# Optimization experiments

Hardware: AMD Instinct MI355X
Metric: run time of the kernel (lower is better)

Reference implementation:

```python
import jax, jax.numpy as jnp
import numpy as np

N_FEATURES = 60
WINDOW = 64
N_FFT_BINS = WINDOW // 2 + 1  # 33
HIDDEN = 256
N_OUT = 3
TOTAL_IN = N_FEATURES + N_FEATURES * N_FFT_BINS  # 2040


def setup_inputs() -> dict:
    key = jax.random.key(0)
    ks = jax.random.split(key, 9)
    B, T = 4, 4096
    x = jax.random.normal(ks[0], (B, T, N_FEATURES), dtype=jnp.float32)

    def lin(k, fan_in, fan_out):
        bound = 1.0 / np.sqrt(fan_in)
        kw, kb = jax.random.split(k)
        W = jax.random.uniform(kw, (fan_in, fan_out), minval=-bound, maxval=bound, dtype=jnp.float32)
        b = jax.random.uniform(kb, (fan_out,), minval=-bound, maxval=bound, dtype=jnp.float32)
        return W, b

    W1, b1 = lin(ks[1], TOTAL_IN, HIDDEN)
    W2, b2 = lin(ks[2], HIDDEN, HIDDEN)
    W3, b3 = lin(ks[3], HIDDEN, HIDDEN // 2)
    W4, b4 = lin(ks[4], HIDDEN // 2, N_OUT)
    return {"x": x, "W1": W1, "b1": b1, "W2": W2, "b2": b2,
            "W3": W3, "b3": b3, "W4": W4, "b4": b4}


def _fft_features(x):
    # x: [B, T, F]
    B, T, F = x.shape
    half_w = WINDOW // 2
    # reflect pad along time: (half_w, half_w - 1)
    xp = jnp.pad(x, ((0, 0), (half_w, half_w - 1), (0, 0)), mode='reflect')  # [B, T+W-1, F]
    # sliding windows: [B, T, W, F] -> [B, T, F, W] (matches torch unfold layout)
    idx = jnp.arange(T)[:, None] + jnp.arange(WINDOW)[None, :]  # [T, W]
    windows = xp[:, idx, :].transpose(0, 1, 3, 2)  # [B, T, F, W]
    fft_mag = jnp.log1p(jnp.abs(jnp.fft.rfft(windows, axis=-1)))  # [B, T, F, W//2+1]
    return fft_mag.reshape(B, T, F * N_FFT_BINS)


def reference(x, W1, b1, W2, b2, W3, b3, W4, b4):
    fft_flat = _fft_features(x)
    h = jnp.concatenate([x, fft_flat], axis=-1)  # [B, T, 2040]
    h = jax.nn.relu(h @ W1 + b1)   # dropout is identity in eval mode
    h = jax.nn.relu(h @ W2 + b2)
    h = jax.nn.relu(h @ W3 + b3)
    return h @ W4 + b4             # [B, T, 3]
```

## Files before the change

### kernel.cpp

```cpp
#include <hip/hip_runtime.h>
#include <math.h>

#define T_LEN 4096
#define NF 60
#define NBINS 33
#define KPAD 2048
#define HID 256
#define NTOK 16384
#define LINE 4160

typedef _Float16 half_t;
typedef half_t half8 __attribute__((ext_vector_type(8)));
typedef half_t half4 __attribute__((ext_vector_type(4)));
typedef float f32x4 __attribute__((ext_vector_type(4)));

constexpr double K_PI = 3.14159265358979323846;
constexpr double tcos(double x) {
    while (x >  K_PI) x -= 2.0 * K_PI;
    while (x < -K_PI) x += 2.0 * K_PI;
    double x2 = x * x, s = 0.0, term = 1.0;
    for (int m = 0; m < 14; ++m) { s += term; term *= -x2 / ((2.0*m + 1.0) * (2.0*m + 2.0)); }
    return s;
}
struct CosTab { float v[64]; };
constexpr CosTab make_tab() {
    CosTab t{};
    for (int j = 0; j < 64; ++j) t.v[j] = (float)tcos(2.0 * K_PI * (double)j / 64.0);
    return t;
}
__device__ constexpr CosTab CTd = make_tab();

__device__ __forceinline__ float log1p_fast(float x) {
    return 0.69314718055994531f * __log2f(1.0f + x);
}

__global__ __launch_bounds__(256) void prep_kernel(
        const float* __restrict__ W1, const float* __restrict__ W2,
        const float* __restrict__ W3,
        half_t* __restrict__ dftH,
        half_t* __restrict__ W1T, half_t* __restrict__ W2T,
        half_t* __restrict__ W3T) {
    int i = blockIdx.x * 256 + threadIdx.x;
    if (i < 4096) {
        int row = i >> 6, n = i & 63;
        float c = (row < 33) ? CTd.v[(row * n) & 63]
                             : CTd.v[((row - 32) * n + 48) & 63];
        dftH[i] = (half_t)c;
        return;
    }
    i -= 4096;
    if (i < 256 * KPAD) {
        int gk = i & (KPAD - 1);
        float v = 0.f;
        if (gk < 2040) {
            int j = i >> 11;
            int r;
            if (gk < 1920) {
                int f = gk >> 5, bin = gk & 31;
                r = NF + f * NBINS + bin;
            } else if (gk < 1980) {
                r = gk - 1920;
            } else {
                r = NF + (gk - 1980) * NBINS + 32;
            }
            v = W1[(size_t)r * HID + j];
        }
        W1T[i] = (half_t)v;
        return;
    }
    i -= 256 * KPAD;
    if (i < 256 * 256) {
        int k = i & 255, j = i >> 8;
        W2T[i] = (half_t)W2[(size_t)k * HID + j];
        return;
    }
    i -= 256 * 256;
    if (i < 128 * 256) {
        int k = i & 255, j = i >> 8;
        W3T[i] = (half_t)W3[(size_t)k * 128 + j];
    }
}

__global__ __launch_bounds__(256) void xline_kernel(
        const float* __restrict__ x, half_t* __restrict__ lineG) {
    const int bf = blockIdx.x;
    const int b = bf / NF, f = bf - b * NF;
    const float* xb = x + (size_t)b * T_LEN * NF + f;
    half_t* L = lineG + (size_t)bf * LINE;
    for (int j = threadIdx.x; j < LINE; j += 256) {
        int s = j - 32;
        int r = (s < 0) ? -s : ((s > T_LEN - 1) ? 2 * (T_LEN - 1) - s : s);
        L[j] = (half_t)xb[(size_t)r * NF];
    }
}

__global__ __launch_bounds__(256) void raw_kernel(
        const float* __restrict__ x, half_t* __restrict__ H0) {
    const int t = blockIdx.x * 256 + threadIdx.x;
    const int b = t >> 12, tl = t & (T_LEN - 1);
    const int i = (b << 12) + ((tl & 7) << 9) + (tl >> 3);
    const float* xp = x + (size_t)t * NF;
    half_t* hp = H0 + (size_t)i * KPAD;
#pragma unroll
    for (int f4 = 0; f4 < 15; ++f4) {
        float4 v = *(const float4*)(xp + f4 * 4);
        half4 h;
        h[0] = (half_t)v.x; h[1] = (half_t)v.y;
        h[2] = (half_t)v.z; h[3] = (half_t)v.w;
        *(half4*)&hp[1920 + f4 * 4] = h;
    }
    half8 z = {};
    *(half8*)&hp[2040] = z;
}

__global__ __launch_bounds__(256) void fft_hankel(
        const half_t* __restrict__ lineG, const half_t* __restrict__ dftH,
        half_t* __restrict__ H0) {
    __shared__ half_t L[LINE];

    const int bid = blockIdx.x;
    const int bf = bid >> 3, c = bid & 7;
    const int b = bf / NF, f = bf - b * NF;
    const int tid = threadIdx.x;
    const int lane = tid & 63, wv = tid >> 6;
    const int lr = lane & 15, lg = lane >> 4;

    half8 a[4][2];
#pragma unroll
    for (int rf = 0; rf < 4; ++rf)
#pragma unroll
        for (int ks = 0; ks < 2; ++ks)
            a[rf][ks] = *(const half8*)&dftH[(16 * rf + lr) * 64 + ks * 32 + lg * 8];

    {
        const half_t* src = lineG + (size_t)bf * LINE + c;
        for (int j = tid; j < 4152; j += 256) L[j] = src[j];
    }
    __syncthreads();

    const int i0 = (b << 12) + (c << 9);

    for (int cs = 0; cs < 8; ++cs) {
        const int s0 = wv * 128 + cs * 16;
        half8 w0 = *(const half8*)&L[8 * (s0 + lr) + lg * 8];
        half8 w1 = *(const half8*)&L[8 * (s0 + lr) + 32 + lg * 8];
        f32x4 dacc[4] = {};
#pragma unroll
        for (int rf = 0; rf < 4; ++rf)
            dacc[rf] = __builtin_amdgcn_mfma_f32_16x16x32_f16(a[rf][0], w0, dacc[rf], 0, 0, 0);
#pragma unroll
        for (int rf = 0; rf < 4; ++rf)
            dacc[rf] = __builtin_amdgcn_mfma_f32_16x16x32_f16(a[rf][1], w1, dacc[rf], 0, 0, 0);

        half_t* base = H0 + (size_t)(i0 + s0 + lr) * KPAD;
#pragma unroll
        for (int rf = 0; rf < 2; ++rf) {
            half4 h4;
#pragma unroll
            for (int r = 0; r < 4; ++r) {
                float re = dacc[rf][r];
                float im = dacc[rf + 2][r];
                float v = (rf == 0 && r == 0)
                    ? ((lg == 0) ? log1p_fast(fabsf(re))
                                 : log1p_fast(sqrtf(re * re + im * im)))
                    : log1p_fast(sqrtf(re * re + im * im));
                h4[r] = (half_t)v;
            }
            *(half4*)&base[f * 32 + 16 * rf + 4 * lg] = h4;
        }
        if (lg == 0)
            base[1980 + f] = (half_t)log1p_fast(fabsf(dacc[2][0]));
    }
}

template<int BN, bool OUT_F32>
__global__ __launch_bounds__(256, 2) void gemm_f16(
        const half_t* __restrict__ A, int lda,
        const half_t* __restrict__ BT, int ldb,
        const float* __restrict__ bias,
        half_t* __restrict__ Ch, float* __restrict__ Cf,
        int N, int K) {
    constexpr int BM = 64;
    constexpr int NFR = BN / 64;
    constexpr int BUNITS = BN * 8 / 256;
    __shared__ half_t As[BM][72];
    __shared__ half_t Bs[BN][72];

    const int tid  = threadIdx.x;
    const int row0 = blockIdx.x * BM;
    const int col0 = blockIdx.y * BN;
    const int wv = tid >> 6, lane = tid & 63;
    const int lr = lane & 15, lg = lane >> 4;

    const int arow = tid >> 2, ak = (tid & 3) * 16;
    const half_t* ap = A + (size_t)(row0 + arow) * lda + ak;

    f32x4 acc[4][NFR] = {};

    for (int k0 = 0; k0 < K; k0 += 64) {
        half8 av0 = *(const half8*)(ap + k0);
        half8 av1 = *(const half8*)(ap + k0 + 8);
        half8 bv[BUNITS];
#pragma unroll
        for (int u = 0; u < BUNITS; ++u) {
            int e = tid + u * 256;
            int n = e >> 3, c8 = (e & 7) * 8;
            bv[u] = *(const half8*)(BT + (size_t)(col0 + n) * ldb + k0 + c8);
        }

        __syncthreads();

        *(half8*)&As[arow][ak]     = av0;
        *(half8*)&As[arow][ak + 8] = av1;
#pragma unroll
        for (int u = 0; u < BUNITS; ++u) {
            int e = tid + u * 256;
            int n = e >> 3, c8 = (e & 7) * 8;
            *(half8*)&Bs[n][c8] = bv[u];
        }

        __syncthreads();

#pragma unroll
        for (int ks = 0; ks < 2; ++ks) {
            half8 af[4], bf[NFR];
#pragma unroll
            for (int mf = 0; mf < 4; ++mf)
                af[mf] = *(const half8*)&As[mf * 16 + lr][ks * 32 + lg * 8];
#pragma unroll
            for (int nf = 0; nf < NFR; ++nf)
                bf[nf] = *(const half8*)&Bs[wv * (16 * NFR) + nf * 16 + lr][ks * 32 + lg * 8];
#pragma unroll
            for (int mf = 0; mf < 4; ++mf)
#pragma unroll
                for (int nf = 0; nf < NFR; ++nf)
                    acc[mf][nf] = __builtin_amdgcn_mfma_f32_16x16x32_f16(af[mf], bf[nf], acc[mf][nf], 0, 0, 0);
        }
    }

#pragma unroll
    for (int nf = 0; nf < NFR; ++nf) {
        int col = col0 + wv * (16 * NFR) + nf * 16 + lr;
        float bs = bias[col];
#pragma unroll
        for (int mf = 0; mf < 4; ++mf)
#pragma unroll
            for (int r = 0; r < 4; ++r) {
                int row = row0 + mf * 16 + lg * 4 + r;
                float v = fmaxf(acc[mf][nf][r] + bs, 0.f);
                if (OUT_F32) Cf[(size_t)row * N + col] = v;
                else         Ch[(size_t)row * N + col] = (half_t)v;
            }
    }
}

__global__ __launch_bounds__(256) void head_kernel(
        const float* __restrict__ H, const float* __restrict__ W4,
        const float* __restrict__ b4, float* __restrict__ out) {
    __shared__ float Ws[128 * 3];
    __shared__ float bs[3];
    for (int i = threadIdx.x; i < 384; i += 256) Ws[i] = W4[i];
    if (threadIdx.x < 3) bs[threadIdx.x] = b4[threadIdx.x];
    __syncthreads();
    const int i = blockIdx.x * 256 + threadIdx.x;
    const float* h = H + (size_t)i * 128;
    float a0 = bs[0], a1 = bs[1], a2 = bs[2];
#pragma unroll
    for (int k = 0; k < 128; ++k) {
        float hv = h[k];
        a0 = fmaf(hv, Ws[k * 3 + 0], a0);
        a1 = fmaf(hv, Ws[k * 3 + 1], a1);
        a2 = fmaf(hv, Ws[k * 3 + 2], a2);
    }
    const int b = i >> 12, c = (i >> 9) & 7, s = i & 511;
    const int t = (b << 12) + (s << 3) + c;
    float* o = out + (size_t)t * 3;
    o[0] = a0; o[1] = a1; o[2] = a2;
}

extern "C" void kernel_launch(void* const* d_in, const int* in_sizes, int n_in,
                              void* d_out, int out_size, void* d_ws, size_t ws_size,
                              hipStream_t stream) {
    (void)in_sizes; (void)n_in; (void)out_size; (void)ws_size;
    const float* x  = (const float*)d_in[0];
    const float* W1 = (const float*)d_in[1];
    const float* b1 = (const float*)d_in[2];
    const float* W2 = (const float*)d_in[3];
    const float* b2 = (const float*)d_in[4];
    const float* W3 = (const float*)d_in[5];
    const float* b3 = (const float*)d_in[6];
    const float* W4 = (const float*)d_in[7];
    const float* b4 = (const float*)d_in[8];
    float* out = (float*)d_out;

    char* w = (char*)d_ws;
    half_t* H0    = (half_t*)(w);
    half_t* H1    = (half_t*)(w + (size_t)64 * 1024 * 1024);
    half_t* H2    = (half_t*)(w + (size_t)72 * 1024 * 1024);
    float*  H3    = (float*) (w + (size_t)80 * 1024 * 1024);
    half_t* W1T   = (half_t*)(w + (size_t)88 * 1024 * 1024);
    half_t* W2T   = (half_t*)(w + (size_t)89 * 1024 * 1024);
    half_t* W3T   = W2T + 256 * 256;
    half_t* dftH  = W3T + 128 * 256;
    half_t* lineG = (half_t*)(w + (size_t)90 * 1024 * 1024);

    prep_kernel<<<2448, 256, 0, stream>>>(W1, W2, W3, dftH, W1T, W2T, W3T);
    xline_kernel<<<240, 256, 0, stream>>>(x, lineG);
    raw_kernel<<<NTOK / 256, 256, 0, stream>>>(x, H0);
    fft_hankel<<<240 * 8, 256, 0, stream>>>(lineG, dftH, H0);

    gemm_f16<128, false><<<dim3(NTOK / 64, 2), 256, 0, stream>>>(
        H0, KPAD, W1T, KPAD, b1, H1, nullptr, HID, KPAD);
    gemm_f16<128, false><<<dim3(NTOK / 64, 2), 256, 0, stream>>>(
        H1, HID, W2T, HID, b2, H2, nullptr, HID, HID);
    gemm_f16<64, true><<<dim3(NTOK / 64, 2), 256, 0, stream>>>(
        H2, HID, W3T, HID, b3, nullptr, H3, HID / 2, HID);

    head_kernel<<<NTOK / 256, 256, 0, stream>>>(H3, W4, b4, out);
}
```

Measured before the change: 107.2 us.

## Split FFT blocks in half, fold ln2 into W1, shrink GEMM1 M-tile

Each fft_hankel block now covers half of its previous token range, which doubles the grid and halves shared memory per block. The line stride grows to 4208, presumably so the second half's reads stay inside each line. The ln(2) factor of log1p moves out of the per-element FFT epilogue and into the FFT rows of W1T during weight prep. The first GEMM moves to a 32-row M tile to launch more blocks. The cost is more blocks and more repeated B-tile loads per output row in GEMM1.

Measured after the change: 119.9 us. +11.8%, slower.

```diff
diff --git a/kernel.cpp b/kernel.cpp
--- a/kernel.cpp
+++ b/kernel.cpp
@@ -7,7 +7,7 @@
 #define KPAD 2048
 #define HID 256
 #define NTOK 16384
-#define LINE 4160
+#define LINE 4208
 
 typedef _Float16 half_t;
 typedef half_t half8 __attribute__((ext_vector_type(8)));
@@ -30,8 +30,8 @@
 }
 __device__ constexpr CosTab CTd = make_tab();
 
-__device__ __forceinline__ float log1p_fast(float x) {
-    return 0.69314718055994531f * __log2f(1.0f + x);
+__device__ __forceinline__ float log2_1p(float x) {
+    return __log2f(1.0f + x);
 }
 
 __global__ __launch_bounds__(256) void prep_kernel(
@@ -55,15 +55,17 @@
         if (gk < 2040) {
             int j = i >> 11;
             int r;
+            bool isfft = true;
             if (gk < 1920) {
                 int f = gk >> 5, bin = gk & 31;
                 r = NF + f * NBINS + bin;
             } else if (gk < 1980) {
-                r = gk - 1920;
+                r = gk - 1920; isfft = false;
             } else {
                 r = NF + (gk - 1980) * NBINS + 32;
             }
             v = W1[(size_t)r * HID + j];
+            if (isfft) v *= 0.69314718055994531f;
         }
         W1T[i] = (half_t)v;
         return;
@@ -116,10 +118,10 @@
 __global__ __launch_bounds__(256) void fft_hankel(
         const half_t* __restrict__ lineG, const half_t* __restrict__ dftH,
         half_t* __restrict__ H0) {
-    __shared__ half_t L[LINE];
+    __shared__ half_t L[2176];
 
     const int bid = blockIdx.x;
-    const int bf = bid >> 3, c = bid & 7;
+    const int bf = bid >> 4, c = (bid >> 1) & 7, hf = bid & 1;
     const int b = bf / NF, f = bf - b * NF;
     const int tid = threadIdx.x;
     const int lane = tid & 63, wv = tid >> 6;
@@ -133,15 +135,16 @@
             a[rf][ks] = *(const half8*)&dftH[(16 * rf + lr) * 64 + ks * 32 + lg * 8];
 
     {
-        const half_t* src = lineG + (size_t)bf * LINE + c;
-        for (int j = tid; j < 4152; j += 256) L[j] = src[j];
+        const half_t* src = lineG + (size_t)bf * LINE + hf * 2048 + c;
+        for (int j = tid; j < 2144; j += 256) L[j] = src[j];
     }
     __syncthreads();
 
-    const int i0 = (b << 12) + (c << 9);
-
-    for (int cs = 0; cs < 8; ++cs) {
-        const int s0 = wv * 128 + cs * 16;
+    const int i0 = (b << 12) + (c << 9) + (hf << 8);
+
+#pragma unroll
+    for (int cs = 0; cs < 4; ++cs) {
+        const int s0 = wv * 64 + cs * 16;
         half8 w0 = *(const half8*)&L[8 * (s0 + lr) + lg * 8];
         half8 w1 = *(const half8*)&L[8 * (s0 + lr) + 32 + lg * 8];
         f32x4 dacc[4] = {};
@@ -161,26 +164,26 @@
                 float re = dacc[rf][r];
                 float im = dacc[rf + 2][r];
                 float v = (rf == 0 && r == 0)
-                    ? ((lg == 0) ? log1p_fast(fabsf(re))
-                                 : log1p_fast(sqrtf(re * re + im * im)))
-                    : log1p_fast(sqrtf(re * re + im * im));
+                    ? ((lg == 0) ? log2_1p(fabsf(re))
+                                 : log2_1p(sqrtf(re * re + im * im)))
+                    : log2_1p(sqrtf(re * re + im * im));
                 h4[r] = (half_t)v;
             }
             *(half4*)&base[f * 32 + 16 * rf + 4 * lg] = h4;
         }
         if (lg == 0)
-            base[1980 + f] = (half_t)log1p_fast(fabsf(dacc[2][0]));
-    }
-}
-
-template<int BN, bool OUT_F32>
+            base[1980 + f] = (half_t)log2_1p(fabsf(dacc[2][0]));
+    }
+}
+
+template<int BM, int BN, bool OUT_F32>
 __global__ __launch_bounds__(256, 2) void gemm_f16(
         const half_t* __restrict__ A, int lda,
         const half_t* __restrict__ BT, int ldb,
         const float* __restrict__ bias,
         half_t* __restrict__ Ch, float* __restrict__ Cf,
         int N, int K) {
-    constexpr int BM = 64;
+    constexpr int MFR = BM / 16;
     constexpr int NFR = BN / 64;
     constexpr int BUNITS = BN * 8 / 256;
     __shared__ half_t As[BM][72];
@@ -192,14 +195,19 @@
     const int wv = tid >> 6, lane = tid & 63;
     const int lr = lane & 15, lg = lane >> 4;
 
-    const int arow = tid >> 2, ak = (tid & 3) * 16;
-    const half_t* ap = A + (size_t)(row0 + arow) * lda + ak;
-
-    f32x4 acc[4][NFR] = {};
+    f32x4 acc[MFR][NFR] = {};
 
     for (int k0 = 0; k0 < K; k0 += 64) {
-        half8 av0 = *(const half8*)(ap + k0);
-        half8 av1 = *(const half8*)(ap + k0 + 8);
+        half8 av0, av1;
+        if (BM == 64) {
+            const int arow = tid >> 2, ak = (tid & 3) * 16;
+            const half_t* ap = A + (size_t)(row0 + arow) * lda + ak + k0;
+            av0 = *(const half8*)ap;
+            av1 = *(const half8*)(ap + 8);
+        } else {
+            const int arow = tid >> 3, ak = (tid & 7) * 8;
+            av0 = *(const half8*)(A + (size_t)(row0 + arow) * lda + ak + k0);
+        }
         half8 bv[BUNITS];
 #pragma unroll
         for (int u = 0; u < BUNITS; ++u) {
@@ -210,8 +218,14 @@
 
         __syncthreads();
 
-        *(half8*)&As[arow][ak]     = av0;
-        *(half8*)&As[arow][ak + 8] = av1;
+        if (BM == 64) {
+            const int arow = tid >> 2, ak = (tid & 3) * 16;
+            *(half8*)&As[arow][ak]     = av0;
+            *(half8*)&As[arow][ak + 8] = av1;
+        } else {
+            const int arow = tid >> 3, ak = (tid & 7) * 8;
+            *(half8*)&As[arow][ak] = av0;
+        }
 #pragma unroll
         for (int u = 0; u < BUNITS; ++u) {
             int e = tid + u * 256;
@@ -223,15 +237,15 @@
 
 #pragma unroll
         for (int ks = 0; ks < 2; ++ks) {
-            half8 af[4], bf[NFR];
-#pragma unroll
-            for (int mf = 0; mf < 4; ++mf)
+            half8 af[MFR], bf[NFR];
+#pragma unroll
+            for (int mf = 0; mf < MFR; ++mf)
                 af[mf] = *(const half8*)&As[mf * 16 + lr][ks * 32 + lg * 8];
 #pragma unroll
             for (int nf = 0; nf < NFR; ++nf)
                 bf[nf] = *(const half8*)&Bs[wv * (16 * NFR) + nf * 16 + lr][ks * 32 + lg * 8];
 #pragma unroll
-            for (int mf = 0; mf < 4; ++mf)
+            for (int mf = 0; mf < MFR; ++mf)
 #pragma unroll
                 for (int nf = 0; nf < NFR; ++nf)
                     acc[mf][nf] = __builtin_amdgcn_mfma_f32_16x16x32_f16(af[mf], bf[nf], acc[mf][nf], 0, 0, 0);
@@ -243,7 +257,7 @@
         int col = col0 + wv * (16 * NFR) + nf * 16 + lr;
         float bs = bias[col];
 #pragma unroll
-        for (int mf = 0; mf < 4; ++mf)
+        for (int mf = 0; mf < MFR; ++mf)
 #pragma unroll
             for (int r = 0; r < 4; ++r) {
                 int row = row0 + mf * 16 + lg * 4 + r;
@@ -307,13 +321,13 @@
     prep_kernel<<<2448, 256, 0, stream>>>(W1, W2, W3, dftH, W1T, W2T, W3T);
     xline_kernel<<<240, 256, 0, stream>>>(x, lineG);
     raw_kernel<<<NTOK / 256, 256, 0, stream>>>(x, H0);
-    fft_hankel<<<240 * 8, 256, 0, stream>>>(lineG, dftH, H0);
-
-    gemm_f16<128, false><<<dim3(NTOK / 64, 2), 256, 0, stream>>>(
+    fft_hankel<<<240 * 16, 256, 0, stream>>>(lineG, dftH, H0);
+
+    gemm_f16<32, 128, false><<<dim3(NTOK / 32, 2), 256, 0, stream>>>(
         H0, KPAD, W1T, KPAD, b1, H1, nullptr, HID, KPAD);
-    gemm_f16<128, false><<<dim3(NTOK / 64, 2), 256, 0, stream>>>(
+    gemm_f16<64, 128, false><<<dim3(NTOK / 64, 2), 256, 0, stream>>>(
         H1, HID, W2T, HID, b2, H2, nullptr, HID, HID);
-    gemm_f16<64, true><<<dim3(NTOK / 64, 2), 256, 0, stream>>>(
+    gemm_f16<64, 64, true><<<dim3(NTOK / 64, 2), 256, 0, stream>>>(
         H2, HID, W3T, HID, b3, nullptr, H3, HID / 2, HID);
 
     head_kernel<<<NTOK / 256, 256, 0, stream>>>(H3, W4, b4, out);
```
